# Kernel optimization log

Hardware: AMD Instinct MI355X
Metric: run time of the kernel (lower is better)

Reference implementation:

```python
import jax, jax.numpy as jnp
import numpy as np

# Padded-CSR SparseLinear: in=out=4096, sparsity=0.9, padding_ratio=0.2
IN_F = 4096
OUT_F = 4096
B = 8192          # flattened leading batch dims
SPARSITY = 0.9
PAD_RATIO = 0.2
NNZ = int(round(IN_F * (1.0 - SPARSITY)))      # 410 live cols per output row
CAP = int(NNZ * (1.0 + PAD_RATIO))             # 492 padded row capacity


def setup_inputs() -> dict:
    key = jax.random.key(0)
    k1, k2, k3, k4 = jax.random.split(key, 4)
    bound = 1.0 / np.sqrt(IN_F)
    x = jax.random.normal(k1, (B, IN_F), dtype=jnp.float32)
    # column indices per padded slot; padded slots point at col 0 with value 0
    col_idx = jax.random.randint(k2, (OUT_F, CAP), 0, IN_F)
    pad_mask = (jnp.arange(CAP) < NNZ).astype(jnp.float32)  # zero out padding slots
    values = jax.random.uniform(k3, (OUT_F, CAP), jnp.float32, -bound, bound) * pad_mask
    bias = jax.random.uniform(k4, (OUT_F,), jnp.float32, -bound, bound)
    return {"x": x, "values": values, "col_idx": col_idx, "bias": bias}


def reference(x, values, col_idx, bias):
    # y[b, o] = sum_k values[o, k] * x[b, col_idx[o, k]] + bias[o]
    # Scan over the padded row-capacity dim so the live intermediate is only [B, OUT_F].
    def step(acc, slot):
        v, c = slot                    # v: [OUT_F] values, c: [OUT_F] column indices
        return acc + x[:, c] * v[None, :], None
    y0 = jnp.zeros((x.shape[0], values.shape[0]), dtype=x.dtype)
    y, _ = jax.lax.scan(step, y0, (values.T, col_idx.T))
    return y + bias[None, :]
```

## Files before the change

### kernel.cpp

```cpp
#include <hip/hip_runtime.h>
#include <hip/hip_bf16.h>
#include <stdint.h>

#define IN_F   4096
#define OUT_F  4096
#define BATCH  8192
#define CAP    492

typedef __bf16 v8bf __attribute__((ext_vector_type(8)));
typedef __bf16 v4bf __attribute__((ext_vector_type(4)));
typedef float  v4f  __attribute__((ext_vector_type(4)));

#define GPTR(p) ((const __attribute__((address_space(1))) void*)(p))
#define LPTR(p) ((__attribute__((address_space(3))) void*)(p))

__global__ __launch_bounds__(256) void convert_kernel(
    const float4* __restrict__ X4,
    v4bf* __restrict__ Xb4)
{
    const int t = threadIdx.x;
    const size_t base = (size_t)blockIdx.x * 8192 + t;
    #pragma unroll
    for (int u = 0; u < 4; ++u) {
        float4 f[8];
        #pragma unroll
        for (int j = 0; j < 8; ++j)
            f[j] = X4[base + (size_t)(u * 8 + j) * 256];
        #pragma unroll
        for (int j = 0; j < 8; ++j) {
            v4bf o;
            o[0] = (__bf16)f[j].x; o[1] = (__bf16)f[j].y;
            o[2] = (__bf16)f[j].z; o[3] = (__bf16)f[j].w;
            Xb4[base + (size_t)(u * 8 + j) * 256] = o;
        }
    }
}

__global__ __launch_bounds__(256) void densify_kernel(
    const float* __restrict__ values,
    const int* __restrict__ col_idx,
    __hip_bfloat16* __restrict__ W)
{
    __shared__ float rowf[2 * IN_F];
    const int t = threadIdx.x;

    #pragma unroll
    for (int i = 0; i < (2 * IN_F) / 256; ++i)
        rowf[t + i * 256] = 0.0f;
    __syncthreads();

    const int r    = t >> 7;
    const int j    = t & 127;
    const int o    = blockIdx.x * 2 + r;
    const int base = o * CAP;
    for (int k = j; k < CAP; k += 128) {
        float v = values[base + k];
        int   c = col_idx[base + k];
        if (v != 0.0f)
            atomicAdd(&rowf[r * IN_F + c], v);
    }
    __syncthreads();

    __hip_bfloat162* W2 = reinterpret_cast<__hip_bfloat162*>(W)
                        + (size_t)blockIdx.x * IN_F;
    #pragma unroll
    for (int i = 0; i < IN_F / 256; ++i) {
        int idx = t + i * 256;
        __hip_bfloat162 h2;
        h2.x = __float2bfloat16(rowf[2 * idx]);
        h2.y = __float2bfloat16(rowf[2 * idx + 1]);
        W2[idx] = h2;
    }
}

__global__ __launch_bounds__(256) void gemm_bias_kernel(
    const __hip_bfloat16* __restrict__ X,
    const __hip_bfloat16* __restrict__ W,
    const float* __restrict__ bias,
    float* __restrict__ Y)
{
    __shared__ uint4 smem[2048];

    const int t    = threadIdx.x;
    const int wave = t >> 6;
    const int lane = t & 63;
    const int ml   = lane & 15;
    const int q    = lane >> 4;
    const int wm   = wave >> 1;
    const int wn   = wave & 1;
    const int bm   = blockIdx.y;
    const int bn   = blockIdx.x;

    const int trow = t >> 3;
    const int k8s  = (t & 7) ^ (trow & 7);
    const __hip_bfloat16* gA = X + (size_t)(bm * 128 + trow) * IN_F + k8s * 8;
    const __hip_bfloat16* gB = W + (size_t)(bn * 128 + trow) * IN_F + k8s * 8;

    const int xr = ml & 7;
    int aBase[4], bBase[4];
    #pragma unroll
    for (int mb = 0; mb < 4; ++mb) aBase[mb] = (wm * 64 + mb * 16 + ml) * 8;
    #pragma unroll
    for (int nf = 0; nf < 4; ++nf) bBase[nf] = 1024 + (wn * 64 + nf * 16 + ml) * 8;

    v4f acc[4][4] = {};

    for (int kt = 0; kt < IN_F / 64; ++kt) {
        const __hip_bfloat16* pa = gA + kt * 64;
        const __hip_bfloat16* pb = gB + kt * 64;
        #pragma unroll
        for (int c = 0; c < 4; ++c)
            __builtin_amdgcn_global_load_lds(GPTR(pa + (size_t)c * 32 * IN_F),
                                             LPTR(&smem[c * 256 + wave * 64]), 16, 0, 0);
        #pragma unroll
        for (int c = 0; c < 4; ++c)
            __builtin_amdgcn_global_load_lds(GPTR(pb + (size_t)c * 32 * IN_F),
                                             LPTR(&smem[1024 + c * 256 + wave * 64]), 16, 0, 0);
        __syncthreads();

        #pragma unroll
        for (int j = 0; j < 2; ++j) {
            const int ko = (j * 4 + q) ^ xr;
            v8bf a[4], b[4];
            #pragma unroll
            for (int mb = 0; mb < 4; ++mb)
                a[mb] = *reinterpret_cast<const v8bf*>(&smem[aBase[mb] + ko]);
            #pragma unroll
            for (int nf = 0; nf < 4; ++nf)
                b[nf] = *reinterpret_cast<const v8bf*>(&smem[bBase[nf] + ko]);
            #pragma unroll
            for (int mb = 0; mb < 4; ++mb)
                #pragma unroll
                for (int nf = 0; nf < 4; ++nf)
                    acc[mb][nf] = __builtin_amdgcn_mfma_f32_16x16x32_bf16(
                        a[mb], b[nf], acc[mb][nf], 0, 0, 0);
        }
        __syncthreads();
    }

    float bf[4];
    #pragma unroll
    for (int nf = 0; nf < 4; ++nf)
        bf[nf] = bias[bn * 128 + wn * 64 + nf * 16 + ml];

    #pragma unroll
    for (int mb = 0; mb < 4; ++mb) {
        const int row0 = bm * 128 + wm * 64 + mb * 16 + q * 4;
        #pragma unroll
        for (int nf = 0; nf < 4; ++nf) {
            const int col = bn * 128 + wn * 64 + nf * 16 + ml;
            float* yp = Y + (size_t)row0 * OUT_F + col;
            #pragma unroll
            for (int r = 0; r < 4; ++r)
                yp[(size_t)r * OUT_F] = acc[mb][nf][r] + bf[nf];
        }
    }
}

__global__ __launch_bounds__(256) void fallback_kernel(
    const float* __restrict__ x,
    const float* __restrict__ values,
    const int* __restrict__ col_idx,
    const float* __restrict__ bias,
    float* __restrict__ y)
{
    __shared__ float xrow[IN_F];
    const int b = blockIdx.y;
    const int t = threadIdx.x;
    for (int i = t; i < IN_F; i += 256)
        xrow[i] = x[(size_t)b * IN_F + i];
    __syncthreads();
    const int o    = blockIdx.x * 256 + t;
    const int base = o * CAP;
    float acc = bias[o];
    for (int k = 0; k < CAP; ++k)
        acc += values[base + k] * xrow[col_idx[base + k]];
    y[(size_t)b * OUT_F + o] = acc;
}

extern "C" void kernel_launch(void* const* d_in, const int* in_sizes, int n_in,
                              void* d_out, int out_size, void* d_ws, size_t ws_size,
                              hipStream_t stream)
{
    const float* x      = (const float*)d_in[0];
    const float* values = (const float*)d_in[1];
    const int*   colidx = (const int*)d_in[2];
    const float* bias   = (const float*)d_in[3];
    float*       y      = (float*)d_out;

    const size_t w_bytes  = (size_t)OUT_F * IN_F * sizeof(__hip_bfloat16);
    const size_t xb_bytes = (size_t)BATCH * IN_F * sizeof(__hip_bfloat16);
    if (ws_size >= w_bytes + xb_bytes) {
        __hip_bfloat16* W  = (__hip_bfloat16*)d_ws;
        __hip_bfloat16* Xb = (__hip_bfloat16*)((char*)d_ws + w_bytes);

        convert_kernel<<<(BATCH * IN_F / 4) / 8192, 256, 0, stream>>>(
            (const float4*)x, (v4bf*)Xb);
        densify_kernel<<<OUT_F / 2, 256, 0, stream>>>(values, colidx, W);

        dim3 grid(OUT_F / 128, BATCH / 128);
        gemm_bias_kernel<<<grid, 256, 0, stream>>>(Xb, W, bias, y);
    } else {
        dim3 grid(OUT_F / 256, BATCH);
        fallback_kernel<<<grid, 256, 0, stream>>>(x, values, colidx, bias, y);
    }
}
```

Measured before the change: 489.7 us.

## Use 256x256 GEMM tiles with double-buffered LDS prefetch and swizzled block order

Reworks the bf16 GEMM to use 512-thread blocks computing 256x256 output tiles, with each wave holding an 8x4 set of MFMA accumulators. The next K-tile is loaded into a second LDS buffer while the current one is consumed, using partial vmcnt waits and raw barriers in place of full syncthreads. Block indices are remapped so neighbouring blocks reuse the same operand tiles in L2, and MFMA sections run at raised wave priority. The goal is to hide global-load latency and raise arithmetic intensity, at the cost of more registers, 128KB of LDS per block and fewer resident blocks.

```diff
diff --git a/kernel.cpp b/kernel.cpp
--- a/kernel.cpp
+++ b/kernel.cpp
@@ -73,86 +73,137 @@
     }
 }
 
-__global__ __launch_bounds__(256) void gemm_bias_kernel(
+__global__ __launch_bounds__(512, 2) void gemm_bias_kernel(
     const __hip_bfloat16* __restrict__ X,
     const __hip_bfloat16* __restrict__ W,
     const float* __restrict__ bias,
     float* __restrict__ Y)
 {
-    __shared__ uint4 smem[2048];
+    __shared__ uint4 smem[8192];
 
     const int t    = threadIdx.x;
     const int wave = t >> 6;
     const int lane = t & 63;
     const int ml   = lane & 15;
     const int q    = lane >> 4;
-    const int wm   = wave >> 1;
-    const int wn   = wave & 1;
-    const int bm   = blockIdx.y;
-    const int bn   = blockIdx.x;
-
-    const int trow = t >> 3;
-    const int k8s  = (t & 7) ^ (trow & 7);
-    const __hip_bfloat16* gA = X + (size_t)(bm * 128 + trow) * IN_F + k8s * 8;
-    const __hip_bfloat16* gB = W + (size_t)(bn * 128 + trow) * IN_F + k8s * 8;
-
-    const int xr = ml & 7;
-    int aBase[4], bBase[4];
-    #pragma unroll
-    for (int mb = 0; mb < 4; ++mb) aBase[mb] = (wm * 64 + mb * 16 + ml) * 8;
-    #pragma unroll
-    for (int nf = 0; nf < 4; ++nf) bBase[nf] = 1024 + (wn * 64 + nf * 16 + ml) * 8;
-
-    v4f acc[4][4] = {};
-
-    for (int kt = 0; kt < IN_F / 64; ++kt) {
-        const __hip_bfloat16* pa = gA + kt * 64;
-        const __hip_bfloat16* pb = gB + kt * 64;
-        #pragma unroll
-        for (int c = 0; c < 4; ++c)
-            __builtin_amdgcn_global_load_lds(GPTR(pa + (size_t)c * 32 * IN_F),
-                                             LPTR(&smem[c * 256 + wave * 64]), 16, 0, 0);
-        #pragma unroll
-        for (int c = 0; c < 4; ++c)
-            __builtin_amdgcn_global_load_lds(GPTR(pb + (size_t)c * 32 * IN_F),
-                                             LPTR(&smem[1024 + c * 256 + wave * 64]), 16, 0, 0);
-        __syncthreads();
-
-        #pragma unroll
-        for (int j = 0; j < 2; ++j) {
-            const int ko = (j * 4 + q) ^ xr;
+    const int wm   = wave >> 2;
+    const int wn   = wave & 3;
+    const int xr   = ml & 7;
+
+    const int flat = blockIdx.y * 16 + blockIdx.x;
+    const int u    = (flat & 7) * 64 + (flat >> 3);
+    const int bn   = u >> 5;
+    const int bm   = u & 31;
+
+    const int rbase = t >> 3;
+    const int gsw   = (t & 7) ^ ((t >> 3) & 7);
+    const __hip_bfloat16* gA = X + (size_t)(bm * 256 + rbase) * IN_F + gsw * 8;
+    const __hip_bfloat16* gB = W + (size_t)(bn * 256 + rbase) * IN_F + gsw * 8;
+
+    const int aRow = wm * 1024 + ml * 8;
+    const int bRow = (2 + (wn >> 1)) * 1024 + ((wn & 1) * 64 + ml) * 8;
+
+    v4f acc[8][4] = {};
+
+    #pragma unroll
+    for (int p = 0; p < 4; ++p) {
+        const __hip_bfloat16* src = (p & 1) ? gB : gA;
+        const int reg = (p & 1) * 2 + (p >> 1);
+        const int hof = (p >> 1) * 128;
+        __builtin_amdgcn_global_load_lds(GPTR(src + (size_t)(hof + 0) * IN_F),
+            LPTR(&smem[reg * 1024 + 0 + wave * 64]), 16, 0, 0);
+        __builtin_amdgcn_global_load_lds(GPTR(src + (size_t)(hof + 64) * IN_F),
+            LPTR(&smem[reg * 1024 + 512 + wave * 64]), 16, 0, 0);
+    }
+
+    for (int kt = 0; kt < 63; ++kt) {
+        const int bufb = kt & 1;
+        const __hip_bfloat16* gAk = gA + (kt + 1) * 64;
+        const __hip_bfloat16* gBk = gB + (kt + 1) * 64;
+        #pragma unroll
+        for (int p = 0; p < 4; ++p) {
+            {
+                const __hip_bfloat16* src = (p & 1) ? gBk : gAk;
+                const int reg = (bufb ^ 1) * 4 + (p & 1) * 2 + (p >> 1);
+                const int hof = (p >> 1) * 128;
+                __builtin_amdgcn_global_load_lds(GPTR(src + (size_t)(hof + 0) * IN_F),
+                    LPTR(&smem[reg * 1024 + 0 + wave * 64]), 16, 0, 0);
+                __builtin_amdgcn_global_load_lds(GPTR(src + (size_t)(hof + 64) * IN_F),
+                    LPTR(&smem[reg * 1024 + 512 + wave * 64]), 16, 0, 0);
+            }
+            if (p == 0) {
+                asm volatile("s_waitcnt vmcnt(2)" ::: "memory");
+                __builtin_amdgcn_sched_barrier(0);
+                __builtin_amdgcn_s_barrier();
+            }
+            const int kg = ((p >> 1) * 4 + q) ^ xr;
             v8bf a[4], b[4];
             #pragma unroll
-            for (int mb = 0; mb < 4; ++mb)
-                a[mb] = *reinterpret_cast<const v8bf*>(&smem[aBase[mb] + ko]);
-            #pragma unroll
-            for (int nf = 0; nf < 4; ++nf)
-                b[nf] = *reinterpret_cast<const v8bf*>(&smem[bBase[nf] + ko]);
-            #pragma unroll
-            for (int mb = 0; mb < 4; ++mb)
+            for (int i = 0; i < 4; ++i)
+                a[i] = *reinterpret_cast<const v8bf*>(
+                    &smem[bufb * 4096 + aRow + ((p & 1) * 4 + i) * 128 + kg]);
+            #pragma unroll
+            for (int j = 0; j < 4; ++j)
+                b[j] = *reinterpret_cast<const v8bf*>(
+                    &smem[bufb * 4096 + bRow + j * 128 + kg]);
+            __builtin_amdgcn_s_setprio(1);
+            #pragma unroll
+            for (int i = 0; i < 4; ++i)
                 #pragma unroll
-                for (int nf = 0; nf < 4; ++nf)
-                    acc[mb][nf] = __builtin_amdgcn_mfma_f32_16x16x32_bf16(
-                        a[mb], b[nf], acc[mb][nf], 0, 0, 0);
-        }
-        __syncthreads();
-    }
-
-    float bf[4];
+                for (int j = 0; j < 4; ++j)
+                    acc[(p & 1) * 4 + i][j] = __builtin_amdgcn_mfma_f32_16x16x32_bf16(
+                        a[i], b[j], acc[(p & 1) * 4 + i][j], 0, 0, 0);
+            __builtin_amdgcn_s_setprio(0);
+            __builtin_amdgcn_s_barrier();
+        }
+    }
+
+    {
+        const int bufb = 1;
+        #pragma unroll
+        for (int p = 0; p < 4; ++p) {
+            if (p == 0) {
+                asm volatile("s_waitcnt vmcnt(0)" ::: "memory");
+                __builtin_amdgcn_sched_barrier(0);
+                __builtin_amdgcn_s_barrier();
+            }
+            const int kg = ((p >> 1) * 4 + q) ^ xr;
+            v8bf a[4], b[4];
+            #pragma unroll
+            for (int i = 0; i < 4; ++i)
+                a[i] = *reinterpret_cast<const v8bf*>(
+                    &smem[bufb * 4096 + aRow + ((p & 1) * 4 + i) * 128 + kg]);
+            #pragma unroll
+            for (int j = 0; j < 4; ++j)
+                b[j] = *reinterpret_cast<const v8bf*>(
+                    &smem[bufb * 4096 + bRow + j * 128 + kg]);
+            __builtin_amdgcn_s_setprio(1);
+            #pragma unroll
+            for (int i = 0; i < 4; ++i)
+                #pragma unroll
+                for (int j = 0; j < 4; ++j)
+                    acc[(p & 1) * 4 + i][j] = __builtin_amdgcn_mfma_f32_16x16x32_bf16(
+                        a[i], b[j], acc[(p & 1) * 4 + i][j], 0, 0, 0);
+            __builtin_amdgcn_s_setprio(0);
+            __builtin_amdgcn_s_barrier();
+        }
+    }
+
+    float bf4[4];
     #pragma unroll
     for (int nf = 0; nf < 4; ++nf)
-        bf[nf] = bias[bn * 128 + wn * 64 + nf * 16 + ml];
-
-    #pragma unroll
-    for (int mb = 0; mb < 4; ++mb) {
-        const int row0 = bm * 128 + wm * 64 + mb * 16 + q * 4;
+        bf4[nf] = bias[bn * 256 + wn * 64 + nf * 16 + ml];
+
+    #pragma unroll
+    for (int mf = 0; mf < 8; ++mf) {
+        const int row0 = bm * 256 + wm * 128 + mf * 16 + q * 4;
         #pragma unroll
         for (int nf = 0; nf < 4; ++nf) {
-            const int col = bn * 128 + wn * 64 + nf * 16 + ml;
+            const int col = bn * 256 + wn * 64 + nf * 16 + ml;
             float* yp = Y + (size_t)row0 * OUT_F + col;
             #pragma unroll
             for (int r = 0; r < 4; ++r)
-                yp[(size_t)r * OUT_F] = acc[mb][nf][r] + bf[nf];
+                yp[(size_t)r * OUT_F] = acc[mf][nf][r] + bf4[nf];
         }
     }
 }
@@ -198,8 +249,8 @@
             (const float4*)x, (v4bf*)Xb);
         densify_kernel<<<OUT_F / 2, 256, 0, stream>>>(values, colidx, W);
 
-        dim3 grid(OUT_F / 128, BATCH / 128);
-        gemm_bias_kernel<<<grid, 256, 0, stream>>>(Xb, W, bias, y);
+        dim3 grid(OUT_F / 256, BATCH / 256);
+        gemm_bias_kernel<<<grid, 512, 0, stream>>>(Xb, W, bias, y);
     } else {
         dim3 grid(OUT_F / 256, BATCH);
         fallback_kernel<<<grid, 256, 0, stream>>>(x, values, colidx, bias, y);
```

New measurement: 501.3 us. +2.4%, slower.

## Restructure GEMM into 256x256 tiles with double-buffered async LDS pipeline

Applied to the files above, without the earlier changes.

Rewrites the bf16 MFMA GEMM to use 512-thread blocks computing 256x256 output tiles, with each wave holding a 128x64 accumulator. It double-buffers K-tiles in LDS (128 KB) using global_load_lds prefetch, synchronised by explicit vmcnt waits and barriers. It also adds a new XOR swizzle, s_setprio around the MFMA bursts, and a remapped block order for L2 locality. The aims are to hide global-load latency, cut barrier stalls and raise arithmetic intensity per LDS byte, at the cost of heavier register and LDS pressure.

```diff
diff --git a/kernel.cpp b/kernel.cpp
--- a/kernel.cpp
+++ b/kernel.cpp
@@ -73,86 +73,133 @@
     }
 }
 
-__global__ __launch_bounds__(256) void gemm_bias_kernel(
+
+#define STAGE(nb, kh, ktn)                                                     \
+  {                                                                            \
+    const __hip_bfloat16* sA = gAs + (ktn) * 64 + (kh) * 32;                   \
+    const __hip_bfloat16* sB = gBs + (ktn) * 64 + (kh) * 32;                   \
+    __builtin_amdgcn_global_load_lds(GPTR(sA),                                 \
+        LPTR(&smem[((nb)*4 + (kh))*1024 + 0   + wave*64]), 16, 0, 0);          \
+    __builtin_amdgcn_global_load_lds(GPTR(sA + (size_t)128 * IN_F),            \
+        LPTR(&smem[((nb)*4 + (kh))*1024 + 512 + wave*64]), 16, 0, 0);          \
+    __builtin_amdgcn_global_load_lds(GPTR(sB),                                 \
+        LPTR(&smem[((nb)*4 + 2 + (kh))*1024 + 0   + wave*64]), 16, 0, 0);      \
+    __builtin_amdgcn_global_load_lds(GPTR(sB + (size_t)128 * IN_F),            \
+        LPTR(&smem[((nb)*4 + 2 + (kh))*1024 + 512 + wave*64]), 16, 0, 0);      \
+  }
+
+#define WAITBAR(n)                                                             \
+  {                                                                            \
+    asm volatile("s_waitcnt vmcnt(" #n ")" ::: "memory");                      \
+    __builtin_amdgcn_sched_barrier(0);                                         \
+    __builtin_amdgcn_s_barrier();                                              \
+  }
+
+#define PHASE_PAIR(bb, kh)                                                     \
+  {                                                                            \
+    const int regA = ((bb)*4 + (kh)) * 1024;                                   \
+    const int regB = ((bb)*4 + 2 + (kh)) * 1024;                               \
+    v8bf Bfr[4], Afr[4];                                                       \
+    _Pragma("unroll")                                                          \
+    for (int nf = 0; nf < 4; ++nf)                                             \
+      Bfr[nf] = *reinterpret_cast<const v8bf*>(&smem[regB + bG[nf]]);          \
+    _Pragma("unroll")                                                          \
+    for (int mf = 0; mf < 4; ++mf)                                             \
+      Afr[mf] = *reinterpret_cast<const v8bf*>(&smem[regA + aG[mf]]);          \
+    __builtin_amdgcn_s_setprio(1);                                             \
+    _Pragma("unroll")                                                          \
+    for (int mf = 0; mf < 4; ++mf)                                             \
+      _Pragma("unroll")                                                        \
+      for (int nf = 0; nf < 4; ++nf)                                           \
+        acc[mf][nf] = __builtin_amdgcn_mfma_f32_16x16x32_bf16(                 \
+            Afr[mf], Bfr[nf], acc[mf][nf], 0, 0, 0);                           \
+    __builtin_amdgcn_s_setprio(0);                                             \
+    _Pragma("unroll")                                                          \
+    for (int mf = 0; mf < 4; ++mf)                                             \
+      Afr[mf] = *reinterpret_cast<const v8bf*>(&smem[regA + aG[4 + mf]]);      \
+    __builtin_amdgcn_s_setprio(1);                                             \
+    _Pragma("unroll")                                                          \
+    for (int mf = 0; mf < 4; ++mf)                                             \
+      _Pragma("unroll")                                                        \
+      for (int nf = 0; nf < 4; ++nf)                                           \
+        acc[4 + mf][nf] = __builtin_amdgcn_mfma_f32_16x16x32_bf16(             \
+            Afr[mf], Bfr[nf], acc[4 + mf][nf], 0, 0, 0);                       \
+    __builtin_amdgcn_s_setprio(0);                                             \
+  }
+
+__global__ __launch_bounds__(512, 2) void gemm_bias_kernel(
     const __hip_bfloat16* __restrict__ X,
     const __hip_bfloat16* __restrict__ W,
     const float* __restrict__ bias,
     float* __restrict__ Y)
 {
-    __shared__ uint4 smem[2048];
+    __shared__ uint4 smem[8192];
 
     const int t    = threadIdx.x;
     const int wave = t >> 6;
     const int lane = t & 63;
     const int ml   = lane & 15;
     const int q    = lane >> 4;
-    const int wm   = wave >> 1;
-    const int wn   = wave & 1;
-    const int bm   = blockIdx.y;
-    const int bn   = blockIdx.x;
-
-    const int trow = t >> 3;
-    const int k8s  = (t & 7) ^ (trow & 7);
-    const __hip_bfloat16* gA = X + (size_t)(bm * 128 + trow) * IN_F + k8s * 8;
-    const __hip_bfloat16* gB = W + (size_t)(bn * 128 + trow) * IN_F + k8s * 8;
-
-    const int xr = ml & 7;
-    int aBase[4], bBase[4];
-    #pragma unroll
-    for (int mb = 0; mb < 4; ++mb) aBase[mb] = (wm * 64 + mb * 16 + ml) * 8;
-    #pragma unroll
-    for (int nf = 0; nf < 4; ++nf) bBase[nf] = 1024 + (wn * 64 + nf * 16 + ml) * 8;
-
-    v4f acc[4][4] = {};
-
-    for (int kt = 0; kt < IN_F / 64; ++kt) {
-        const __hip_bfloat16* pa = gA + kt * 64;
-        const __hip_bfloat16* pb = gB + kt * 64;
-        #pragma unroll
-        for (int c = 0; c < 4; ++c)
-            __builtin_amdgcn_global_load_lds(GPTR(pa + (size_t)c * 32 * IN_F),
-                                             LPTR(&smem[c * 256 + wave * 64]), 16, 0, 0);
-        #pragma unroll
-        for (int c = 0; c < 4; ++c)
-            __builtin_amdgcn_global_load_lds(GPTR(pb + (size_t)c * 32 * IN_F),
-                                             LPTR(&smem[1024 + c * 256 + wave * 64]), 16, 0, 0);
-        __syncthreads();
-
-        #pragma unroll
-        for (int j = 0; j < 2; ++j) {
-            const int ko = (j * 4 + q) ^ xr;
-            v8bf a[4], b[4];
-            #pragma unroll
-            for (int mb = 0; mb < 4; ++mb)
-                a[mb] = *reinterpret_cast<const v8bf*>(&smem[aBase[mb] + ko]);
-            #pragma unroll
-            for (int nf = 0; nf < 4; ++nf)
-                b[nf] = *reinterpret_cast<const v8bf*>(&smem[bBase[nf] + ko]);
-            #pragma unroll
-            for (int mb = 0; mb < 4; ++mb)
-                #pragma unroll
-                for (int nf = 0; nf < 4; ++nf)
-                    acc[mb][nf] = __builtin_amdgcn_mfma_f32_16x16x32_bf16(
-                        a[mb], b[nf], acc[mb][nf], 0, 0, 0);
-        }
-        __syncthreads();
-    }
-
-    float bf[4];
+    const int wm   = wave >> 2;
+    const int wn   = wave & 3;
+
+    const int flat = blockIdx.y * 16 + blockIdx.x;
+    const int u    = (flat & 7) * 64 + (flat >> 3);
+    const int bn   = u >> 5;
+    const int bm   = u & 31;
+
+    const int srow = t >> 2;
+    const int sg   = (t & 3) ^ ((srow + (srow >> 2)) & 3);
+    const __hip_bfloat16* gAs = X + (size_t)(bm * 256 + srow) * IN_F + sg * 8;
+    const __hip_bfloat16* gBs = W + (size_t)(bn * 256 + srow) * IN_F + sg * 8;
+
+    int aG[8], bG[4];
+    #pragma unroll
+    for (int mf = 0; mf < 8; ++mf) {
+        const int ar = wm * 128 + mf * 16 + ml;
+        aG[mf] = ar * 4 + (q ^ ((ar + (ar >> 2)) & 3));
+    }
+    #pragma unroll
+    for (int nf = 0; nf < 4; ++nf) {
+        const int br = wn * 64 + nf * 16 + ml;
+        bG[nf] = br * 4 + (q ^ ((br + (br >> 2)) & 3));
+    }
+
+    v4f acc[8][4] = {};
+
+    STAGE(0, 0, 0);
+    STAGE(0, 1, 0);
+
+    for (int kt = 0; kt < 63; ++kt) {
+        const int bb = kt & 1;
+        const int nb = bb ^ 1;
+        STAGE(nb, 0, kt + 1);
+        WAITBAR(8);
+        if (bb) { PHASE_PAIR(1, 0); } else { PHASE_PAIR(0, 0); }
+        STAGE(nb, 1, kt + 1);
+        WAITBAR(8);
+        if (bb) { PHASE_PAIR(1, 1); } else { PHASE_PAIR(0, 1); }
+    }
+    WAITBAR(4);
+    PHASE_PAIR(1, 0);
+    WAITBAR(0);
+    PHASE_PAIR(1, 1);
+
+    float bf4[4];
     #pragma unroll
     for (int nf = 0; nf < 4; ++nf)
-        bf[nf] = bias[bn * 128 + wn * 64 + nf * 16 + ml];
-
-    #pragma unroll
-    for (int mb = 0; mb < 4; ++mb) {
-        const int row0 = bm * 128 + wm * 64 + mb * 16 + q * 4;
+        bf4[nf] = bias[bn * 256 + wn * 64 + nf * 16 + ml];
+
+    #pragma unroll
+    for (int mf = 0; mf < 8; ++mf) {
+        const int row0 = bm * 256 + wm * 128 + mf * 16 + q * 4;
         #pragma unroll
         for (int nf = 0; nf < 4; ++nf) {
-            const int col = bn * 128 + wn * 64 + nf * 16 + ml;
+            const int col = bn * 256 + wn * 64 + nf * 16 + ml;
             float* yp = Y + (size_t)row0 * OUT_F + col;
             #pragma unroll
             for (int r = 0; r < 4; ++r)
-                yp[(size_t)r * OUT_F] = acc[mb][nf][r] + bf[nf];
+                yp[(size_t)r * OUT_F] = acc[mf][nf][r] + bf4[nf];
         }
     }
 }
@@ -198,8 +245,8 @@
             (const float4*)x, (v4bf*)Xb);
         densify_kernel<<<OUT_F / 2, 256, 0, stream>>>(values, colidx, W);
 
-        dim3 grid(OUT_F / 128, BATCH / 128);
-        gemm_bias_kernel<<<grid, 256, 0, stream>>>(Xb, W, bias, y);
+        dim3 grid(OUT_F / 256, BATCH / 256);
+        gemm_bias_kernel<<<grid, 512, 0, stream>>>(Xb, W, bias, y);
     } else {
         dim3 grid(OUT_F / 256, BATCH);
         fallback_kernel<<<grid, 256, 0, stream>>>(x, values, colidx, bias, y);
```

Result: slower. 845.4 us (+72.6%).
